# Performance work log

Measured on AMD Instinct MI355X. Metric: run time of the kernel, lower is better.

The kernel has to match this reference:

```python
import jax, jax.numpy as jnp
import numpy as np

B, T, C, H = 8, 2048, 1024, 16
S = C // H
LN_EPS = 1e-5


def setup_inputs() -> dict:
    key = jax.random.key(0)
    ks = jax.random.split(key, 12)
    w = lambda k: jax.random.normal(k, (C, C), dtype=jnp.float32) * 0.02
    return {
        "x": jax.random.normal(ks[0], (B, T, C), dtype=jnp.float32),
        "time_mix_k": jax.random.uniform(ks[1], (1, 1, C), dtype=jnp.float32),
        "time_mix_v": jax.random.uniform(ks[2], (1, 1, C), dtype=jnp.float32),
        "time_mix_r": jax.random.uniform(ks[3], (1, 1, C), dtype=jnp.float32),
        # keep exp(time_decay) < 1 for numerical stability over T=2048 steps
        "time_decay": -jax.random.uniform(ks[4], (H, S), minval=0.1, maxval=5.0, dtype=jnp.float32),
        "time_first": jax.random.uniform(ks[5], (H, S), dtype=jnp.float32),
        "Wk": w(ks[6]), "Wv": w(ks[7]), "Wr": w(ks[8]), "Wo": w(ks[9]),
        "ln_g": jnp.ones((C,), jnp.float32),
        "ln_b": jnp.zeros((C,), jnp.float32),
    }


def reference(x, time_mix_k, time_mix_v, time_mix_r, time_decay, time_first, Wk, Wv, Wr, Wo, ln_g, ln_b):
    Bx, Tx, Cx = x.shape
    # time_shift: xx[t] = x[t-1], xx[0] = 0
    xx = jnp.pad(x, ((0, 0), (1, 0), (0, 0)))[:, :-1]
    xk = x * time_mix_k + xx * (1 - time_mix_k)
    xv = x * time_mix_v + xx * (1 - time_mix_v)
    xr = x * time_mix_r + xx * (1 - time_mix_r)
    proj = lambda z, W: jnp.einsum('btc,dc->btd', z, W).reshape(Bx, Tx, H, S)
    k = proj(xk, Wk)  # [B,T,H,S]
    v = proj(xv, Wv)
    r = proj(xr, Wr)
    kv = k * v  # elementwise per-channel 'at' (diagonal of outer-product state)
    decay = jnp.exp(time_decay)  # [H,S]

    def step(state, inp):
        kv_t, r_t = inp  # [B,H,S] each
        state = kv_t + decay * state
        o = r_t * (time_first * kv_t + state)
        return state, o

    kvT = jnp.swapaxes(kv, 0, 1)  # [T,B,H,S]
    rT = jnp.swapaxes(r, 0, 1)
    _, outT = jax.lax.scan(step, jnp.zeros((Bx, H, S), x.dtype), (kvT, rT))
    out = jnp.swapaxes(outT, 0, 1).reshape(Bx, Tx, Cx)
    mu = out.mean(-1, keepdims=True)
    var = out.var(-1, keepdims=True)
    out = (out - mu) / jnp.sqrt(var + LN_EPS) * ln_g + ln_b
    return jnp.einsum('btc,dc->btd', out, Wo)
```

## Files before the change

### kernel.cpp

```cpp
#include <hip/hip_runtime.h>

#define Bsz 8
#define Tn  2048
#define Cn  1024
#define Hn  16
#define Sn  64
#define Mn  (Bsz * Tn)
#define NC  32
#define LCH (Tn / NC)
#define Kd  1024
#define NKT (Kd / 64)

typedef __attribute__((ext_vector_type(8))) short bf16x8;
typedef __attribute__((ext_vector_type(4))) float f32x4;

__device__ __forceinline__ unsigned short f2bf(float f) {
  union { float f; unsigned int u; } v;
  v.f = f;
  unsigned int r = (v.u + 0x7FFFu + ((v.u >> 16) & 1u)) >> 16;
  return (unsigned short)r;
}
__device__ __forceinline__ float bf2f(unsigned short u) {
  union { unsigned int u; float f; } v;
  v.u = ((unsigned int)u) << 16;
  return v.f;
}

__global__ void wconv_kernel(const float* __restrict__ Wk, const float* __restrict__ Wv,
                             const float* __restrict__ Wr, const float* __restrict__ Wo,
                             unsigned short* __restrict__ out) {
  int i = blockIdx.x * blockDim.x + threadIdx.x;
  int which = i >> 18;
  int off = (i & 0x3FFFF) * 4;
  const float* src = which == 0 ? Wk : which == 1 ? Wv : which == 2 ? Wr : Wo;
  float4 f = *(const float4*)(src + off);
  ushort4 o;
  o.x = f2bf(f.x); o.y = f2bf(f.y); o.z = f2bf(f.z); o.w = f2bf(f.w);
  *(ushort4*)(out + (size_t)which * (Cn * Cn) + off) = o;
}

__global__ void mix3_kernel(const float* __restrict__ x,
                            const float* __restrict__ tmk, const float* __restrict__ tmv,
                            const float* __restrict__ tmr,
                            unsigned short* __restrict__ ok, unsigned short* __restrict__ ov,
                            unsigned short* __restrict__ orr) {
  int idx = blockIdx.x * blockDim.x + threadIdx.x;
  int c4 = idx & (Cn / 4 - 1);
  int bt = idx >> 8;
  int t = bt & (Tn - 1);
  size_t base = (size_t)bt * Cn + c4 * 4;
  float4 xv = *(const float4*)(x + base);
  float4 xxv = {0.f, 0.f, 0.f, 0.f};
  if (t != 0) xxv = *(const float4*)(x + base - Cn);
  float4 dx = {xv.x - xxv.x, xv.y - xxv.y, xv.z - xxv.z, xv.w - xxv.w};
  float4 tk = *(const float4*)(tmk + c4 * 4);
  float4 tv = *(const float4*)(tmv + c4 * 4);
  float4 tr = *(const float4*)(tmr + c4 * 4);
  ushort4 a, b, c;
  a.x = f2bf(xxv.x + tk.x * dx.x); a.y = f2bf(xxv.y + tk.y * dx.y);
  a.z = f2bf(xxv.z + tk.z * dx.z); a.w = f2bf(xxv.w + tk.w * dx.w);
  b.x = f2bf(xxv.x + tv.x * dx.x); b.y = f2bf(xxv.y + tv.y * dx.y);
  b.z = f2bf(xxv.z + tv.z * dx.z); b.w = f2bf(xxv.w + tv.w * dx.w);
  c.x = f2bf(xxv.x + tr.x * dx.x); c.y = f2bf(xxv.y + tr.y * dx.y);
  c.z = f2bf(xxv.z + tr.z * dx.z); c.w = f2bf(xxv.w + tr.w * dx.w);
  *(ushort4*)(ok + base) = a;
  *(ushort4*)(ov + base) = b;
  *(ushort4*)(orr + base) = c;
}

__device__ __forceinline__ void gload_lds16(const void* g, void* l) {
  __builtin_amdgcn_global_load_lds((const __attribute__((address_space(1))) void*)g,
                                   (__attribute__((address_space(3))) void*)l, 16, 0, 0);
}

#define PHASE(H, KS, LOADB, PRE, POST)                                             \
  {                                                                                \
    _Pragma("unroll") for (int mi4 = 0; mi4 < 4; ++mi4) {                          \
      const int row = wm * 128 + (H) * 64 + mi4 * 16 + l15;                        \
      aF[mi4] = *(const bf16x8*)(ldsc + dbase + row * 128 +                        \
                                 ((((KS) * 4 + lg) ^ (row & 7)) << 4));            \
    }                                                                              \
    if (LOADB) {                                                                   \
      _Pragma("unroll") for (int nj = 0; nj < 4; ++nj) {                           \
        const int row = wn * 64 + nj * 16 + l15;                                   \
        bF[nj] = *(const bf16x8*)(ldsc + dbase + 32768 + row * 128 +               \
                                  ((((KS) * 4 + lg) ^ (row & 7)) << 4));           \
      }                                                                            \
    }                                                                              \
    PRE;                                                                           \
    __builtin_amdgcn_s_barrier();                                                  \
    asm volatile("s_waitcnt lgkmcnt(0)" ::: "memory");                             \
    __builtin_amdgcn_sched_barrier(0);                                             \
    __builtin_amdgcn_s_setprio(1);                                                 \
    _Pragma("unroll") for (int mi4 = 0; mi4 < 4; ++mi4)                            \
      _Pragma("unroll") for (int nj = 0; nj < 4; ++nj)                             \
        acc[(H) * 4 + mi4][nj] = __builtin_amdgcn_mfma_f32_16x16x32_bf16(          \
            aF[mi4], bF[nj], acc[(H) * 4 + mi4][nj], 0, 0, 0);                     \
    __builtin_amdgcn_s_setprio(0);                                                 \
    POST;                                                                          \
    __builtin_amdgcn_s_barrier();                                                  \
  }

template <bool OUTBF16>
__global__ __launch_bounds__(512, 2) void gemm8p(const unsigned short* __restrict__ A,
                                                 const unsigned short* __restrict__ Bt,
                                                 void* __restrict__ Cm) {
  __shared__ unsigned short lds[65536];
  char* ldsc = (char*)lds;
  const int tid = threadIdx.x;
  const int wid = tid >> 6, lane = tid & 63;
  const int wm = wid >> 2, wn = wid & 3;
  const int l15 = lane & 15, lg = lane >> 4;
  int bid = ((int)blockIdx.x & 7) * 32 + ((int)blockIdx.x >> 3);
  const int mt = bid >> 2, nt = bid & 3;
  const int m0 = mt * 256, n0 = nt * 256;

  const unsigned short* Ag = A + (size_t)m0 * Kd;
  const unsigned short* Bg = Bt + (size_t)n0 * Kd;

  auto stageSlice = [&](const unsigned short* gbase, int ktt, int band, int Loff) {
    const int r = band * 64 + wid * 8 + (lane >> 3);
    const int c = (lane & 7) ^ (r & 7);
    gload_lds16(gbase + (size_t)r * Kd + ktt * 64 + c * 8,
                ldsc + Loff + (band * 64 + wid * 8) * 128 + lane * 16);
  };
  auto stage8 = [&](int ktt, int base) {
    stageSlice(Bg, ktt, 0, base + 32768);
    stageSlice(Bg, ktt, 1, base + 32768);
    stageSlice(Bg, ktt, 2, base + 32768);
    stageSlice(Bg, ktt, 3, base + 32768);
    stageSlice(Ag, ktt, 0, base);
    stageSlice(Ag, ktt, 2, base);
    stageSlice(Ag, ktt, 1, base);
    stageSlice(Ag, ktt, 3, base);
  };

  f32x4 acc[8][4] = {};
  bf16x8 aF[4], bF[4];

  stage8(0, 0);
  asm volatile("s_waitcnt vmcnt(2)" ::: "memory");
  __builtin_amdgcn_s_barrier();

  for (int kt = 0; kt < NKT; ++kt) {
    const int dbase = (kt & 1) << 16;
    const int nd = dbase ^ 65536;
    const bool st = (kt + 1 < NKT);
    PHASE(0, 0, 1, ;, asm volatile("s_waitcnt vmcnt(0)" ::: "memory"))
    PHASE(1, 0, 0, if (st) stage8(kt + 1, nd), ;)
    PHASE(1, 1, 1, ;, ;)
    PHASE(0, 1, 0, ;, asm volatile("s_waitcnt vmcnt(2)" ::: "memory"))
  }

  if (OUTBF16) {
    char* tb = ldsc + wid * 16384;
#pragma unroll
    for (int mi = 0; mi < 8; ++mi)
#pragma unroll
      for (int nj = 0; nj < 4; ++nj)
#pragma unroll
        for (int rr = 0; rr < 4; ++rr) {
          const int row = mi * 16 + lg * 4 + rr;
          const int col = nj * 16 + l15;
          *(unsigned short*)(tb + row * 128 + ((col * 2) ^ ((row & 7) << 4))) =
              f2bf(acc[mi][nj][rr]);
        }
    asm volatile("s_waitcnt lgkmcnt(0)" ::: "memory");
    __builtin_amdgcn_sched_barrier(0);
    const int orl = lane >> 3, och = lane & 7;
#pragma unroll
    for (int it = 0; it < 16; ++it) {
      const int row = it * 8 + orl;
      uint4 vv = *(const uint4*)(tb + row * 128 + ((och * 16) ^ ((row & 7) << 4)));
      const int gr = m0 + wm * 128 + row;
      const int gc = n0 + wn * 64 + och * 8;
      *(uint4*)((unsigned short*)Cm + (size_t)gr * Cn + gc) = vv;
    }
  } else {
#pragma unroll
    for (int mi = 0; mi < 8; ++mi)
#pragma unroll
      for (int nj = 0; nj < 4; ++nj)
#pragma unroll
        for (int rr = 0; rr < 4; ++rr) {
          const int row = m0 + wm * 128 + mi * 16 + lg * 4 + rr;
          const int col = n0 + wn * 64 + nj * 16 + l15;
          ((float*)Cm)[(size_t)row * Cn + col] = acc[mi][nj][rr];
        }
  }
}

__global__ void scan_phase1(const unsigned short* __restrict__ k,
                            const unsigned short* __restrict__ v,
                            const float* __restrict__ td, float* __restrict__ cs) {
  int blk = blockIdx.x;
  int c = blk & (NC - 1);
  int bh = blk >> 5;
  int b = bh >> 4;
  int h = bh & 15;
  int s = threadIdx.x;
  float decay = expf(td[h * Sn + s]);
  size_t base = ((size_t)(b * Tn + c * LCH)) * Cn + h * Sn + s;
  float st = 0.f;
#pragma unroll 8
  for (int i = 0; i < LCH; ++i) {
    float kv = bf2f(k[base]) * bf2f(v[base]);
    st = kv + decay * st;
    base += Cn;
  }
  cs[(size_t)blk * Sn + s] = st;
}

__global__ void scan_phase2(const float* __restrict__ td, float* __restrict__ cs) {
  int bh = blockIdx.x;
  int h = bh & 15;
  int s = threadIdx.x;
  float dL = expf(td[h * Sn + s] * (float)LCH);
  float carry = 0.f;
  for (int c = 0; c < NC; ++c) {
    size_t idx = ((size_t)bh * NC + c) * Sn + s;
    float sc = cs[idx];
    cs[idx] = carry;
    carry = sc + dL * carry;
  }
}

__global__ void scan_phase3(const unsigned short* __restrict__ k,
                            const unsigned short* __restrict__ v,
                            const unsigned short* __restrict__ r,
                            const float* __restrict__ td, const float* __restrict__ tf,
                            const float* __restrict__ cs,
                            unsigned short* __restrict__ out) {
  int blk = blockIdx.x;
  int c = blk & (NC - 1);
  int bh = blk >> 5;
  int b = bh >> 4;
  int h = bh & 15;
  int s = threadIdx.x;
  float decay = expf(td[h * Sn + s]);
  float first = tf[h * Sn + s];
  float st = cs[(size_t)blk * Sn + s];
  size_t base = ((size_t)(b * Tn + c * LCH)) * Cn + h * Sn + s;
#pragma unroll 8
  for (int i = 0; i < LCH; ++i) {
    float kv = bf2f(k[base]) * bf2f(v[base]);
    st = kv + decay * st;
    out[base] = f2bf(bf2f(r[base]) * (first * kv + st));
    base += Cn;
  }
}

__global__ __launch_bounds__(256) void ln_kernel(const unsigned short* __restrict__ in,
                                                 const float* __restrict__ g,
                                                 const float* __restrict__ bb,
                                                 unsigned short* __restrict__ out) {
  int row = blockIdx.x;
  int tid = threadIdx.x;
  size_t base = (size_t)row * Cn + tid * 4;
  ushort4 uv = *(const ushort4*)(in + base);
  float4 xv = {bf2f(uv.x), bf2f(uv.y), bf2f(uv.z), bf2f(uv.w)};
  float sum = xv.x + xv.y + xv.z + xv.w;
  float ss = xv.x * xv.x + xv.y * xv.y + xv.z * xv.z + xv.w * xv.w;
#pragma unroll
  for (int off = 32; off >= 1; off >>= 1) {
    sum += __shfl_down(sum, off, 64);
    ss += __shfl_down(ss, off, 64);
  }
  __shared__ float s1[4], s2[4];
  if ((tid & 63) == 0) { s1[tid >> 6] = sum; s2[tid >> 6] = ss; }
  __syncthreads();
  sum = s1[0] + s1[1] + s1[2] + s1[3];
  ss = s2[0] + s2[1] + s2[2] + s2[3];
  float mu = sum * (1.f / Cn);
  float var = ss * (1.f / Cn) - mu * mu;
  float rstd = rsqrtf(var + 1e-5f);
  float4 gv = *(const float4*)(g + tid * 4);
  float4 bv = *(const float4*)(bb + tid * 4);
  ushort4 o;
  o.x = f2bf((xv.x - mu) * rstd * gv.x + bv.x);
  o.y = f2bf((xv.y - mu) * rstd * gv.y + bv.y);
  o.z = f2bf((xv.z - mu) * rstd * gv.z + bv.z);
  o.w = f2bf((xv.w - mu) * rstd * gv.w + bv.w);
  *(ushort4*)(out + base) = o;
}

extern "C" void kernel_launch(void* const* d_in, const int* in_sizes, int n_in,
                              void* d_out, int out_size, void* d_ws, size_t ws_size,
                              hipStream_t stream) {
  const float* x   = (const float*)d_in[0];
  const float* tmk = (const float*)d_in[1];
  const float* tmv = (const float*)d_in[2];
  const float* tmr = (const float*)d_in[3];
  const float* td  = (const float*)d_in[4];
  const float* tf  = (const float*)d_in[5];
  const float* Wk  = (const float*)d_in[6];
  const float* Wv  = (const float*)d_in[7];
  const float* Wr  = (const float*)d_in[8];
  const float* Wo  = (const float*)d_in[9];
  const float* lng = (const float*)d_in[10];
  const float* lnb = (const float*)d_in[11];
  float* out = (float*)d_out;

  char* ws = (char*)d_ws;
  const size_t MB = 1024 * 1024;
  unsigned short* wbf  = (unsigned short*)(ws);
  unsigned short* xk   = (unsigned short*)(ws + 8 * MB);
  unsigned short* xv_  = (unsigned short*)(ws + 40 * MB);
  unsigned short* xr   = (unsigned short*)(ws + 72 * MB);
  unsigned short* bufK = (unsigned short*)(ws + 104 * MB);
  unsigned short* bufV = (unsigned short*)(ws + 136 * MB);
  unsigned short* bufR = (unsigned short*)(ws + 168 * MB);
  unsigned short* preLN = xk;
  unsigned short* lnout = xv_;
  float* chunkS = (float*)(ws + 200 * MB);

  const int gemm_grid = (Mn / 256) * (Cn / 256);
  const int mix_grid = Mn * (Cn / 4) / 256;

  wconv_kernel<<<4 * Cn * Cn / 4 / 256, 256, 0, stream>>>(Wk, Wv, Wr, Wo, wbf);
  mix3_kernel<<<mix_grid, 256, 0, stream>>>(x, tmk, tmv, tmr, xk, xv_, xr);

  gemm8p<true><<<gemm_grid, 512, 0, stream>>>(xk,  wbf + 0 * (size_t)Cn * Cn, bufK);
  gemm8p<true><<<gemm_grid, 512, 0, stream>>>(xv_, wbf + 1 * (size_t)Cn * Cn, bufV);
  gemm8p<true><<<gemm_grid, 512, 0, stream>>>(xr,  wbf + 2 * (size_t)Cn * Cn, bufR);

  scan_phase1<<<Bsz * Hn * NC, 64, 0, stream>>>(bufK, bufV, td, chunkS);
  scan_phase2<<<Bsz * Hn, 64, 0, stream>>>(td, chunkS);
  scan_phase3<<<Bsz * Hn * NC, 64, 0, stream>>>(bufK, bufV, bufR, td, tf, chunkS, preLN);

  ln_kernel<<<Mn, 256, 0, stream>>>(preLN, lng, lnb, lnout);

  gemm8p<false><<<gemm_grid, 512, 0, stream>>>(lnout, wbf + 3 * (size_t)Cn * Cn, out);

  (void)in_sizes; (void)n_in; (void)out_size; (void)ws_size;
}
```

Baseline: 257.5 us.

## Replace eight-phase GEMM schedule with single-barrier-per-tile double-buffered loop

Swaps the hand-interleaved four-phase-per-k-tile GEMM main loop for a simpler loop with one barrier per tile. The loop prefetches the next k-tile into the other LDS buffer up front, then interleaves LDS fragment reads with MFMA groups in straight-line code. It drops the explicit vmcnt/lgkmcnt waits, the setprio hints and the mid-tile barriers, and relies on __syncthreads and the compiler scheduler instead. The aim is less barrier overhead, at the cost of losing fine-grained control over the overlap between memory and MFMA work.

```diff
diff --git a/kernel.cpp b/kernel.cpp
--- a/kernel.cpp
+++ b/kernel.cpp
@@ -73,36 +73,26 @@
                                    (__attribute__((address_space(3))) void*)l, 16, 0, 0);
 }
 
-#define PHASE(H, KS, LOADB, PRE, POST)                                             \
-  {                                                                                \
-    _Pragma("unroll") for (int mi4 = 0; mi4 < 4; ++mi4) {                          \
-      const int row = wm * 128 + (H) * 64 + mi4 * 16 + l15;                        \
-      aF[mi4] = *(const bf16x8*)(ldsc + dbase + row * 128 +                        \
-                                 ((((KS) * 4 + lg) ^ (row & 7)) << 4));            \
-    }                                                                              \
-    if (LOADB) {                                                                   \
-      _Pragma("unroll") for (int nj = 0; nj < 4; ++nj) {                           \
-        const int row = wn * 64 + nj * 16 + l15;                                   \
-        bF[nj] = *(const bf16x8*)(ldsc + dbase + 32768 + row * 128 +               \
-                                  ((((KS) * 4 + lg) ^ (row & 7)) << 4));           \
-      }                                                                            \
-    }                                                                              \
-    PRE;                                                                           \
-    __builtin_amdgcn_s_barrier();                                                  \
-    asm volatile("s_waitcnt lgkmcnt(0)" ::: "memory");                             \
-    __builtin_amdgcn_sched_barrier(0);                                             \
-    __builtin_amdgcn_s_setprio(1);                                                 \
-    _Pragma("unroll") for (int mi4 = 0; mi4 < 4; ++mi4)                            \
-      _Pragma("unroll") for (int nj = 0; nj < 4; ++nj)                             \
-        acc[(H) * 4 + mi4][nj] = __builtin_amdgcn_mfma_f32_16x16x32_bf16(          \
-            aF[mi4], bF[nj], acc[(H) * 4 + mi4][nj], 0, 0, 0);                     \
-    __builtin_amdgcn_s_setprio(0);                                                 \
-    POST;                                                                          \
-    __builtin_amdgcn_s_barrier();                                                  \
-  }
+#define LDA(dst, H, KS)                                                            \
+  _Pragma("unroll") for (int mi4 = 0; mi4 < 4; ++mi4) {                            \
+    const int row = wm * 128 + (H) * 64 + mi4 * 16 + l15;                          \
+    dst[mi4] = *(const bf16x8*)(ldsc + dbase + row * 128 +                         \
+                                ((((KS) * 4 + lg) ^ (row & 7)) << 4));             \
+  }
+#define LDB(dst, KS)                                                               \
+  _Pragma("unroll") for (int nj = 0; nj < 4; ++nj) {                               \
+    const int row = wn * 64 + nj * 16 + l15;                                       \
+    dst[nj] = *(const bf16x8*)(ldsc + dbase + 32768 + row * 128 +                  \
+                               ((((KS) * 4 + lg) ^ (row & 7)) << 4));              \
+  }
+#define MFMA16(H, AV, BV)                                                          \
+  _Pragma("unroll") for (int mi4 = 0; mi4 < 4; ++mi4)                              \
+    _Pragma("unroll") for (int nj = 0; nj < 4; ++nj)                               \
+      acc[(H) * 4 + mi4][nj] = __builtin_amdgcn_mfma_f32_16x16x32_bf16(            \
+          AV[mi4], BV[nj], acc[(H) * 4 + mi4][nj], 0, 0, 0);
 
 template <bool OUTBF16>
-__global__ __launch_bounds__(512, 2) void gemm8p(const unsigned short* __restrict__ A,
+__global__ __launch_bounds__(512, 2) void gemm1b(const unsigned short* __restrict__ A,
                                                  const unsigned short* __restrict__ Bt,
                                                  void* __restrict__ Cm) {
   __shared__ unsigned short lds[65536];
@@ -125,31 +115,36 @@
                 ldsc + Loff + (band * 64 + wid * 8) * 128 + lane * 16);
   };
   auto stage8 = [&](int ktt, int base) {
-    stageSlice(Bg, ktt, 0, base + 32768);
-    stageSlice(Bg, ktt, 1, base + 32768);
-    stageSlice(Bg, ktt, 2, base + 32768);
-    stageSlice(Bg, ktt, 3, base + 32768);
-    stageSlice(Ag, ktt, 0, base);
-    stageSlice(Ag, ktt, 2, base);
-    stageSlice(Ag, ktt, 1, base);
-    stageSlice(Ag, ktt, 3, base);
+#pragma unroll
+    for (int band = 0; band < 4; ++band) stageSlice(Ag, ktt, band, base);
+#pragma unroll
+    for (int band = 0; band < 4; ++band) stageSlice(Bg, ktt, band, base + 32768);
   };
 
   f32x4 acc[8][4] = {};
-  bf16x8 aF[4], bF[4];
 
   stage8(0, 0);
-  asm volatile("s_waitcnt vmcnt(2)" ::: "memory");
-  __builtin_amdgcn_s_barrier();
-
+  __syncthreads();
+
+#pragma unroll 2
   for (int kt = 0; kt < NKT; ++kt) {
     const int dbase = (kt & 1) << 16;
     const int nd = dbase ^ 65536;
-    const bool st = (kt + 1 < NKT);
-    PHASE(0, 0, 1, ;, asm volatile("s_waitcnt vmcnt(0)" ::: "memory"))
-    PHASE(1, 0, 0, if (st) stage8(kt + 1, nd), ;)
-    PHASE(1, 1, 1, ;, ;)
-    PHASE(0, 1, 0, ;, asm volatile("s_waitcnt vmcnt(2)" ::: "memory"))
+    if (kt + 1 < NKT) stage8(kt + 1, nd);
+
+    bf16x8 a0[4], a1[4], a2[4], a3[4], b0[4], b1[4];
+    LDA(a0, 0, 0)
+    LDB(b0, 0)
+    LDA(a1, 1, 0)
+    MFMA16(0, a0, b0)
+    LDA(a2, 1, 1)
+    LDB(b1, 1)
+    MFMA16(1, a1, b0)
+    LDA(a3, 0, 1)
+    MFMA16(1, a2, b1)
+    MFMA16(0, a3, b1)
+
+    __syncthreads();
   }
 
   if (OUTBF16) {
@@ -320,9 +315,9 @@
   wconv_kernel<<<4 * Cn * Cn / 4 / 256, 256, 0, stream>>>(Wk, Wv, Wr, Wo, wbf);
   mix3_kernel<<<mix_grid, 256, 0, stream>>>(x, tmk, tmv, tmr, xk, xv_, xr);
 
-  gemm8p<true><<<gemm_grid, 512, 0, stream>>>(xk,  wbf + 0 * (size_t)Cn * Cn, bufK);
-  gemm8p<true><<<gemm_grid, 512, 0, stream>>>(xv_, wbf + 1 * (size_t)Cn * Cn, bufV);
-  gemm8p<true><<<gemm_grid, 512, 0, stream>>>(xr,  wbf + 2 * (size_t)Cn * Cn, bufR);
+  gemm1b<true><<<gemm_grid, 512, 0, stream>>>(xk,  wbf + 0 * (size_t)Cn * Cn, bufK);
+  gemm1b<true><<<gemm_grid, 512, 0, stream>>>(xv_, wbf + 1 * (size_t)Cn * Cn, bufV);
+  gemm1b<true><<<gemm_grid, 512, 0, stream>>>(xr,  wbf + 2 * (size_t)Cn * Cn, bufR);
 
   scan_phase1<<<Bsz * Hn * NC, 64, 0, stream>>>(bufK, bufV, td, chunkS);
   scan_phase2<<<Bsz * Hn, 64, 0, stream>>>(td, chunkS);
@@ -330,7 +325,7 @@
 
   ln_kernel<<<Mn, 256, 0, stream>>>(preLN, lng, lnb, lnout);
 
-  gemm8p<false><<<gemm_grid, 512, 0, stream>>>(lnout, wbf + 3 * (size_t)Cn * Cn, out);
+  gemm1b<false><<<gemm_grid, 512, 0, stream>>>(lnout, wbf + 3 * (size_t)Cn * Cn, out);
 
   (void)in_sizes; (void)n_in; (void)out_size; (void)ws_size;
 }
```

Result: faster. 252.1 us (-2.1%).
